# Optimization experiments

Measured on AMD Instinct MI355X. Metric: run time of the kernel, lower is better.

## Reference

```python
import jax, jax.numpy as jnp
import numpy as np

K0, K1, K2, D, DIM, H = 200_000, 600_000, 400_000, 64, 3, 256


def setup_inputs() -> dict:
    key = jax.random.key(0)
    ks = jax.random.split(key, 7)
    dirs = jax.random.normal(ks[0], (D, DIM), dtype=jnp.float32)
    dirs = dirs / jnp.linalg.norm(dirs, axis=1, keepdims=True)  # unit directions
    v_coords = jax.random.normal(ks[1], (K0, DIM), dtype=jnp.float32)
    v_weights = jax.random.uniform(ks[2], (K0,), dtype=jnp.float32)
    edges = jax.random.randint(ks[3], (K1, 2), 0, K0, dtype=jnp.int32)
    e_weights = jax.random.uniform(ks[4], (K1,), dtype=jnp.float32)
    tris = jax.random.randint(ks[5], (K2, 3), 0, K0, dtype=jnp.int32)
    t_weights = jax.random.uniform(ks[6], (K2,), dtype=jnp.float32)
    return dict(v_coords=v_coords, v_weights=v_weights, edges=edges,
                e_weights=e_weights, tris=tris, t_weights=t_weights,
                dirs=dirs, num_heights=H)


def reference(v_coords, v_weights, edges, e_weights, tris, t_weights, dirs, num_heights):
    d = dirs.shape[0]
    h = int(num_heights)
    hf = jnp.asarray(float(h), dtype=v_coords.dtype)
    # vertex height indices per direction: (k0, d)
    max_height = jnp.linalg.norm(v_coords, axis=1).max()
    v_heights = v_coords @ dirs.T
    v_idx = jnp.ceil((hf - 1.0) * (max_height + v_heights) / (2.0 * max_height)).astype(jnp.int32)
    # flattened (d*h,) histogram; per-direction offset folds (dir, height) -> flat bin
    dir_off = (jnp.arange(d, dtype=jnp.int32) * h)[None, :]  # (1, d)
    flat = jnp.zeros((d * h,), dtype=v_weights.dtype)
    # order 0: vertices, sign +1
    flat = flat.at[(v_idx + dir_off).ravel()].add(
        jnp.broadcast_to(v_weights[:, None], v_idx.shape).ravel())
    # order 1: edges, sign (-1)**(1+1) = +1; max vertex index over the 2 endpoints
    e_idx = jnp.max(v_idx[edges], axis=1)  # (k1, d)
    flat = flat.at[(e_idx + dir_off).ravel()].add(
        jnp.broadcast_to(e_weights[:, None], e_idx.shape).ravel())
    # order 2: triangles, sign (-1)**(2+1) = -1; max over the 3 vertices
    t_idx = jnp.max(v_idx[tris], axis=1)  # (k2, d)
    flat = flat.at[(t_idx + dir_off).ravel()].add(
        jnp.broadcast_to(-t_weights[:, None], t_idx.shape).ravel())
    # cumulative sum over heights -> WECT, shape (d, h)
    return jnp.cumsum(flat.reshape(d, h), axis=1)
```

## Files before the change

kernel.cpp:

```cpp
#include <hip/hip_runtime.h>


#define HGT 256
#define NDIR 64
#define NBINS (HGT * NDIR)
#define NG 4
#define GD 16
#define PADH16 258
#define WH16 (GD * PADH16)
#define TPB 192
#define NWV (TPB / 64)
#define VSL 384
#define SSL 384
#define UE 2
#define UT 2
#define UV 2
#define QSCALE 32.0f
#define QINV (1.0f / 32.0f)

__global__ void wect_maxnorm(const float* __restrict__ vc, int k0,
                             unsigned* __restrict__ maxbits) {
    float m = 0.f;
    for (int i = blockIdx.x * blockDim.x + threadIdx.x; i < k0;
         i += gridDim.x * blockDim.x) {
        float x = vc[3 * i], y = vc[3 * i + 1], z = vc[3 * i + 2];
        m = fmaxf(m, sqrtf(x * x + y * y + z * z));
    }
    for (int off = 32; off > 0; off >>= 1)
        m = fmaxf(m, __shfl_down(m, off, 64));
    __shared__ float sm[16];
    int wid = threadIdx.x >> 6, lane = threadIdx.x & 63;
    if (lane == 0) sm[wid] = m;
    __syncthreads();
    if (threadIdx.x == 0) {
        float b = sm[0];
        int nw = blockDim.x >> 6;
        for (int w = 1; w < nw; ++w) b = fmaxf(b, sm[w]);
        atomicMax(maxbits, __float_as_uint(b));
    }
}

__device__ __forceinline__ int height_bin(float h, float mh, float inv) {
    int idx = (int)ceilf((255.0f * (mh + h)) * inv);
    return min(max(idx, 0), HGT - 1);
}

__device__ __forceinline__ int haddr(int dl, int b) {
    int p = ((b & 1) << 7) | (b >> 1);
    return dl * PADH16 + p;
}

__device__ __forceinline__ void flush6(const short* hist, int g,
                                       float* __restrict__ out) {
    for (int t = threadIdx.x; t < GD * HGT; t += TPB) {
        int d = t >> 8, b = t & 255;
        int p = d * PADH16 + (((b & 1) << 7) | (b >> 1));
        int s = 0;
#pragma unroll
        for (int u = 0; u < NWV; ++u) s += (int)hist[u * WH16 + p];
        if (s != 0) atomicAdd(&out[(g * GD + d) * HGT + b], (float)s * QINV);
    }
}

__global__ __launch_bounds__(TPB, 4) void wect_vertex4(
    const float* __restrict__ vc, const float* __restrict__ vw,
    const float* __restrict__ dirs, int k0,
    const unsigned* __restrict__ maxbits, unsigned char* __restrict__ tab,
    float* __restrict__ out) {
    __shared__ short hist[NWV * WH16];
    int tid = threadIdx.x, lane = tid & 63, wv = tid >> 6;
    int dl = lane & 15, sub = lane >> 4;
    for (int t = tid; t < NWV * WH16; t += TPB) hist[t] = 0;
    int g = blockIdx.x & (NG - 1);
    int slice = blockIdx.x >> 2;
    int gd = g * GD + dl;
    float dx = dirs[3 * gd], dy = dirs[3 * gd + 1], dz = dirs[3 * gd + 2];
    float mh = __uint_as_float(*maxbits);
    float inv = 1.0f / (2.0f * mh);
    unsigned char* tabg = tab + (size_t)g * ((size_t)k0 * GD);
    short* H = hist + wv * WH16;
    __syncthreads();
    int lo = (int)((long long)k0 * slice / VSL);
    int hi = (int)((long long)k0 * (slice + 1) / VSL);
    for (int s0 = lo + wv * 4 * UV; s0 < hi; s0 += NWV * 4 * UV) {
        int a_[UV];
        int q_[UV];
#pragma unroll
        for (int u = 0; u < UV; ++u) {
            int s = min(s0 + u * 4 + sub, hi - 1);
            bool act = (s0 + u * 4 + sub) < hi;
            float x = vc[3 * s], y = vc[3 * s + 1], z = vc[3 * s + 2];
            float w = act ? vw[s] : 0.f;
            float h = fmaf(x, dx, fmaf(y, dy, z * dz));
            int b = height_bin(h, mh, inv);
            if (act) tabg[(unsigned)s * GD + dl] = (unsigned char)b;
            a_[u] = haddr(dl, b);
            q_[u] = __float2int_rn(w * QSCALE);
        }
#pragma unroll
        for (int ss = 0; ss < 4; ++ss) {
            if (sub == ss) {
#pragma unroll
                for (int u = 0; u < UV; ++u) {
                    short v = H[a_[u]];
                    H[a_[u]] = (short)(v + q_[u]);
                }
            }
            asm volatile("" ::: "memory");
        }
    }
    __syncthreads();
    flush6(hist, g, out);
}

__global__ __launch_bounds__(TPB, 4) void wect_simplex4(
    const long long* __restrict__ edges, const float* __restrict__ ew,
    const int* __restrict__ tris, const float* __restrict__ tw, int k1, int k2,
    const unsigned char* __restrict__ tab, int k0, float* __restrict__ out) {
    __shared__ short hist[NWV * WH16];
    int tid = threadIdx.x, lane = tid & 63, wv = tid >> 6;
    int dl = lane & 15, sub = lane >> 4;
    for (int t = tid; t < NWV * WH16; t += TPB) hist[t] = 0;
    int g = blockIdx.x & (NG - 1);
    int slice = blockIdx.x >> 2;
    const unsigned char* tabg = tab + (size_t)g * ((size_t)k0 * GD);
    short* H = hist + wv * WH16;
    __syncthreads();

    {
        int lo = (int)((long long)k1 * slice / SSL);
        int hi = (int)((long long)k1 * (slice + 1) / SSL);
        for (int s0 = lo + wv * 4 * UE; s0 < hi; s0 += NWV * 4 * UE) {
            int a_[UE];
            int q_[UE];
#pragma unroll
            for (int u = 0; u < UE; ++u) {
                int s = min(s0 + u * 4 + sub, hi - 1);
                bool act = (s0 + u * 4 + sub) < hi;
                long long ep = edges[s];
                float w = act ? ew[s] : 0.f;
                unsigned ex = (unsigned)(ep & 0xffffffffLL);
                unsigned ey = (unsigned)(ep >> 32);
                int A = tabg[ex * GD + dl];
                int B = tabg[ey * GD + dl];
                a_[u] = haddr(dl, max(A, B));
                q_[u] = __float2int_rn(w * QSCALE);
            }
#pragma unroll
            for (int ss = 0; ss < 4; ++ss) {
                if (sub == ss) {
#pragma unroll
                    for (int u = 0; u < UE; ++u) {
                        short v = H[a_[u]];
                        H[a_[u]] = (short)(v + q_[u]);
                    }
                }
                asm volatile("" ::: "memory");
            }
        }
    }

    {
        int lo = (int)((long long)k2 * slice / SSL);
        int hi = (int)((long long)k2 * (slice + 1) / SSL);
        for (int s0 = lo + wv * 4 * UT; s0 < hi; s0 += NWV * 4 * UT) {
            int a_[UT];
            int q_[UT];
#pragma unroll
            for (int u = 0; u < UT; ++u) {
                int s = min(s0 + u * 4 + sub, hi - 1);
                bool act = (s0 + u * 4 + sub) < hi;
                unsigned i0 = (unsigned)tris[3 * s];
                unsigned i1 = (unsigned)tris[3 * s + 1];
                unsigned i2 = (unsigned)tris[3 * s + 2];
                float w = act ? -tw[s] : 0.f;
                int A = tabg[i0 * GD + dl];
                int B = tabg[i1 * GD + dl];
                int C = tabg[i2 * GD + dl];
                a_[u] = haddr(dl, max(A, max(B, C)));
                q_[u] = __float2int_rn(w * QSCALE);
            }
#pragma unroll
            for (int ss = 0; ss < 4; ++ss) {
                if (sub == ss) {
#pragma unroll
                    for (int u = 0; u < UT; ++u) {
                        short v = H[a_[u]];
                        H[a_[u]] = (short)(v + q_[u]);
                    }
                }
                asm volatile("" ::: "memory");
            }
        }
    }

    __syncthreads();
    flush6(hist, g, out);
}

__global__ void wect_cumsum(float* __restrict__ out) {
    int lane = threadIdx.x;
    float4* row = (float4*)out + (size_t)blockIdx.x * 64;
    float4 v = row[lane];
    v.y += v.x;
    v.z += v.y;
    v.w += v.z;
    float s = v.w;
    float mine = s;
    for (int off = 1; off < 64; off <<= 1) {
        float t = __shfl_up(s, off, 64);
        if (lane >= off) s += t;
    }
    float excl = s - mine;
    v.x += excl;
    v.y += excl;
    v.z += excl;
    v.w += excl;
    row[lane] = v;
}


__global__ __launch_bounds__(512) void wect_simplex_rec(
    const int* __restrict__ edges, const float* __restrict__ ew,
    const int* __restrict__ tris, const float* __restrict__ tw, int k1, int k2,
    const float* __restrict__ vc, const float* __restrict__ dirs,
    const unsigned* __restrict__ maxbits, float* __restrict__ out) {
    __shared__ float hist[NBINS];
    for (int i = threadIdx.x; i < NBINS; i += blockDim.x) hist[i] = 0.f;
    int lane = threadIdx.x & 63;
    float d0 = dirs[lane * 3], d1 = dirs[lane * 3 + 1], d2 = dirs[lane * 3 + 2];
    float mh = __uint_as_float(*maxbits);
    float inv = 1.0f / (2.0f * mh);
    __syncthreads();
    int wid = (blockIdx.x * blockDim.x + threadIdx.x) >> 6;
    int nw = (gridDim.x * blockDim.x) >> 6;
    int total = k1 + k2;
    for (int s = wid; s < total; s += nw) {
        int idx;
        float w;
        if (s < k1) {
            int v0 = edges[2 * s], v1 = edges[2 * s + 1];
            float h0 = vc[3 * v0] * d0 + vc[3 * v0 + 1] * d1 + vc[3 * v0 + 2] * d2;
            float h1 = vc[3 * v1] * d0 + vc[3 * v1 + 1] * d1 + vc[3 * v1 + 2] * d2;
            idx = max(height_bin(h0, mh, inv), height_bin(h1, mh, inv));
            w = ew[s];
        } else {
            int t = s - k1;
            int v0 = tris[3 * t], v1 = tris[3 * t + 1], v2 = tris[3 * t + 2];
            float h0 = vc[3 * v0] * d0 + vc[3 * v0 + 1] * d1 + vc[3 * v0 + 2] * d2;
            float h1 = vc[3 * v1] * d0 + vc[3 * v1 + 1] * d1 + vc[3 * v1 + 2] * d2;
            float h2 = vc[3 * v2] * d0 + vc[3 * v2 + 1] * d1 + vc[3 * v2 + 2] * d2;
            idx = max(height_bin(h0, mh, inv),
                      max(height_bin(h1, mh, inv), height_bin(h2, mh, inv)));
            w = -tw[t];
        }
        atomicAdd(&hist[idx * NDIR + lane], w);
    }
    __syncthreads();
    for (int i = threadIdx.x; i < NBINS; i += blockDim.x) {
        float v = hist[i];
        if (v != 0.f) atomicAdd(&out[(i & 63) * HGT + (i >> 6)], v);
    }
}

__global__ __launch_bounds__(512) void wect_vertex_rec(
    const float* __restrict__ vc, const float* __restrict__ vw,
    const float* __restrict__ dirs, int k0,
    const unsigned* __restrict__ maxbits, float* __restrict__ out) {
    __shared__ float hist[NBINS];
    for (int i = threadIdx.x; i < NBINS; i += blockDim.x) hist[i] = 0.f;
    int lane = threadIdx.x & 63;
    float d0 = dirs[lane * 3], d1 = dirs[lane * 3 + 1], d2 = dirs[lane * 3 + 2];
    float mh = __uint_as_float(*maxbits);
    float inv = 1.0f / (2.0f * mh);
    __syncthreads();
    int wid = (blockIdx.x * blockDim.x + threadIdx.x) >> 6;
    int nw = (gridDim.x * blockDim.x) >> 6;
    for (int k = wid; k < k0; k += nw) {
        float h = vc[3 * k] * d0 + vc[3 * k + 1] * d1 + vc[3 * k + 2] * d2;
        int idx = height_bin(h, mh, inv);
        atomicAdd(&hist[idx * NDIR + lane], vw[k]);
    }
    __syncthreads();
    for (int i = threadIdx.x; i < NBINS; i += blockDim.x) {
        float v = hist[i];
        if (v != 0.f) atomicAdd(&out[(i & 63) * HGT + (i >> 6)], v);
    }
}

extern "C" void kernel_launch(void* const* d_in, const int* in_sizes, int n_in,
                              void* d_out, int out_size, void* d_ws,
                              size_t ws_size, hipStream_t stream) {
    const float* v_coords = (const float*)d_in[0];
    const float* v_weights = (const float*)d_in[1];
    const int* edges = (const int*)d_in[2];
    const float* e_weights = (const float*)d_in[3];
    const int* tris = (const int*)d_in[4];
    const float* t_weights = (const float*)d_in[5];
    const float* dirs = (const float*)d_in[6];

    int k0 = in_sizes[0] / 3;
    int k1 = in_sizes[2] / 2;
    int k2 = in_sizes[4] / 3;

    float* out = (float*)d_out;
    unsigned* maxbits = (unsigned*)d_ws;
    unsigned char* tab = (unsigned char*)d_ws + 64;
    bool have_table = ws_size >= 64 + (size_t)NG * k0 * GD;

    (void)hipMemsetAsync(d_ws, 0, 64, stream);
    (void)hipMemsetAsync(d_out, 0, (size_t)NBINS * sizeof(float), stream);

    wect_maxnorm<<<256, 256, 0, stream>>>(v_coords, k0, maxbits);

    if (have_table) {
        wect_vertex4<<<NG * VSL, TPB, 0, stream>>>(v_coords, v_weights, dirs,
                                                   k0, maxbits, tab, out);
        wect_simplex4<<<NG * SSL, TPB, 0, stream>>>(
            (const long long*)edges, e_weights, tris, t_weights, k1, k2, tab,
            k0, out);
    } else {
        wect_vertex_rec<<<512, 512, 0, stream>>>(v_coords, v_weights, dirs, k0,
                                                 maxbits, out);
        wect_simplex_rec<<<512, 512, 0, stream>>>(edges, e_weights, tris,
                                                  t_weights, k1, k2, v_coords,
                                                  dirs, maxbits, out);
    }
    wect_cumsum<<<NDIR, 64, 0, stream>>>(out);
}
```

Before: 218.9 us.

## Replace serialized sub-group histogram updates with cross-lane dedupe and single update

Each wave holds 4 sub-groups of 16 lanes that can hit the same direction's histogram row. The old code avoided read-modify-write races by taking 4 serialized turns, one per sub-group. The new code uses permlane16/32 swaps (or shfl_xor as a fallback) to find lanes with the same bin address, merges their weights into one lane, and sends the rest to a padding slot. All 64 lanes then do one LDS read-modify-write per element. This trades 4 serialized LDS passes for extra cross-lane VALU work, and relies on the padding column at index 256 to absorb the retired lanes.

```diff
diff --git a/kernel.cpp b/kernel.cpp
--- a/kernel.cpp
+++ b/kernel.cpp
@@ -17,6 +17,45 @@
 #define UV 2
 #define QSCALE 32.0f
 #define QINV (1.0f / 32.0f)
+
+typedef __attribute__((ext_vector_type(2))) unsigned int uint2e;
+
+__device__ __forceinline__ int lxor16(int x, int lane) {
+#if __has_builtin(__builtin_amdgcn_permlane16_swap)
+    uint2e r =
+        __builtin_amdgcn_permlane16_swap((unsigned)x, (unsigned)x, false, false);
+    return (int)((lane & 16) ? r[0] : r[1]);
+#else
+    return __shfl_xor(x, 16, 64);
+#endif
+}
+
+__device__ __forceinline__ int lxor32(int x, int lane) {
+#if __has_builtin(__builtin_amdgcn_permlane32_swap)
+    uint2e r =
+        __builtin_amdgcn_permlane32_swap((unsigned)x, (unsigned)x, false, false);
+    return (int)((lane & 32) ? r[0] : r[1]);
+#else
+    return __shfl_xor(x, 32, 64);
+#endif
+}
+
+__device__ __forceinline__ void dedupe_valu(int& a, int& q, int lane, int pad) {
+    int a16 = lxor16(a, lane), q16 = lxor16(q, lane);
+    int a32 = lxor32(a, lane), q32 = lxor32(q, lane);
+    int a48 = lxor16(a32, lane), q48 = lxor16(q32, lane);
+    bool m16 = (a16 == a), m32 = (a32 == a), m48 = (a48 == a);
+    bool hi16 = (lane & 16) != 0, hi32 = (lane & 32) != 0;
+    bool retired = (m16 && hi16) || ((m32 || m48) && hi32);
+    if (retired) {
+        a = pad;
+        q = 0;
+    } else {
+        if (m16 && !hi16) q += q16;
+        if (m32 && !hi32) q += q32;
+        if (m48 && !hi32) q += q48;
+    }
+}
 
 __global__ void wect_maxnorm(const float* __restrict__ vc, int k0,
                              unsigned* __restrict__ maxbits) {
@@ -79,6 +118,7 @@
     float inv = 1.0f / (2.0f * mh);
     unsigned char* tabg = tab + (size_t)g * ((size_t)k0 * GD);
     short* H = hist + wv * WH16;
+    int pad = dl * PADH16 + 256;
     __syncthreads();
     int lo = (int)((long long)k0 * slice / VSL);
     int hi = (int)((long long)k0 * (slice + 1) / VSL);
@@ -98,15 +138,10 @@
             q_[u] = __float2int_rn(w * QSCALE);
         }
 #pragma unroll
-        for (int ss = 0; ss < 4; ++ss) {
-            if (sub == ss) {
-#pragma unroll
-                for (int u = 0; u < UV; ++u) {
-                    short v = H[a_[u]];
-                    H[a_[u]] = (short)(v + q_[u]);
-                }
-            }
-            asm volatile("" ::: "memory");
+        for (int u = 0; u < UV; ++u) {
+            dedupe_valu(a_[u], q_[u], lane, pad);
+            short v = H[a_[u]];
+            H[a_[u]] = (short)(v + q_[u]);
         }
     }
     __syncthreads();
@@ -125,6 +160,7 @@
     int slice = blockIdx.x >> 2;
     const unsigned char* tabg = tab + (size_t)g * ((size_t)k0 * GD);
     short* H = hist + wv * WH16;
+    int pad = dl * PADH16 + 256;
     __syncthreads();
 
     {
@@ -147,15 +183,10 @@
                 q_[u] = __float2int_rn(w * QSCALE);
             }
 #pragma unroll
-            for (int ss = 0; ss < 4; ++ss) {
-                if (sub == ss) {
-#pragma unroll
-                    for (int u = 0; u < UE; ++u) {
-                        short v = H[a_[u]];
-                        H[a_[u]] = (short)(v + q_[u]);
-                    }
-                }
-                asm volatile("" ::: "memory");
+            for (int u = 0; u < UE; ++u) {
+                dedupe_valu(a_[u], q_[u], lane, pad);
+                short v = H[a_[u]];
+                H[a_[u]] = (short)(v + q_[u]);
             }
         }
     }
@@ -181,15 +212,10 @@
                 q_[u] = __float2int_rn(w * QSCALE);
             }
 #pragma unroll
-            for (int ss = 0; ss < 4; ++ss) {
-                if (sub == ss) {
-#pragma unroll
-                    for (int u = 0; u < UT; ++u) {
-                        short v = H[a_[u]];
-                        H[a_[u]] = (short)(v + q_[u]);
-                    }
-                }
-                asm volatile("" ::: "memory");
+            for (int u = 0; u < UT; ++u) {
+                dedupe_valu(a_[u], q_[u], lane, pad);
+                short v = H[a_[u]];
+                H[a_[u]] = (short)(v + q_[u]);
             }
         }
     }
```

Measured after the change: 221.2 us. About the same (+1.1%).

## Replace serialized sub-group histogram updates with cross-lane duplicate merging

Applied to the files above, without the earlier changes.

Previously, each wave's four 16-lane subgroups updated the shared short histogram one after another to avoid read-modify-write collisions. Now lanes that share a direction compare bin addresses through permlane16/32 swaps (falling back to shuffles). Colliding quantized weights are summed into one owner lane, and the other lanes write zero to a pad slot, so all 64 lanes update the histogram in one pass. A full-chunk fast loop without bounds predicates is also split from a tail loop, at the cost of extra packing and permute instructions per update.

```diff
diff --git a/kernel.cpp b/kernel.cpp
--- a/kernel.cpp
+++ b/kernel.cpp
@@ -17,6 +17,46 @@
 #define UV 2
 #define QSCALE 32.0f
 #define QINV (1.0f / 32.0f)
+
+typedef __attribute__((ext_vector_type(2))) unsigned int uint2e;
+
+__device__ __forceinline__ unsigned pxor16(unsigned x, int lane) {
+#if __has_builtin(__builtin_amdgcn_permlane16_swap)
+    uint2e r = __builtin_amdgcn_permlane16_swap(x, x, false, false);
+    return (lane & 16) ? r[0] : r[1];
+#else
+    return (unsigned)__shfl_xor((int)x, 16, 64);
+#endif
+}
+
+__device__ __forceinline__ unsigned pxor32(unsigned x, int lane) {
+#if __has_builtin(__builtin_amdgcn_permlane32_swap)
+    uint2e r = __builtin_amdgcn_permlane32_swap(x, x, false, false);
+    return (lane & 32) ? r[0] : r[1];
+#else
+    return (unsigned)__shfl_xor((int)x, 32, 64);
+#endif
+}
+
+__device__ __forceinline__ void dedupe_pk(int& a, int& q, int lane, int pad) {
+    unsigned p = ((unsigned)a << 16) | ((unsigned)q & 0xffffu);
+    unsigned p16 = pxor16(p, lane);
+    unsigned p32 = pxor32(p, lane);
+    unsigned p48 = pxor16(p32, lane);
+    bool m16 = ((p ^ p16) >> 16) == 0;
+    bool m32 = ((p ^ p32) >> 16) == 0;
+    bool m48 = ((p ^ p48) >> 16) == 0;
+    bool hi16 = (lane & 16) != 0, hi32 = (lane & 32) != 0;
+    bool retired = (m16 && hi16) || ((m32 || m48) && hi32);
+    if (retired) {
+        a = pad;
+        q = 0;
+    } else {
+        if (m16 && !hi16) q += (short)(p16 & 0xffffu);
+        if (m32 && !hi32) q += (short)(p32 & 0xffffu);
+        if (m48 && !hi32) q += (short)(p48 & 0xffffu);
+    }
+}
 
 __global__ void wect_maxnorm(const float* __restrict__ vc, int k0,
                              unsigned* __restrict__ maxbits) {
@@ -79,12 +119,33 @@
     float inv = 1.0f / (2.0f * mh);
     unsigned char* tabg = tab + (size_t)g * ((size_t)k0 * GD);
     short* H = hist + wv * WH16;
+    int pad = dl * PADH16 + 256;
     __syncthreads();
     int lo = (int)((long long)k0 * slice / VSL);
     int hi = (int)((long long)k0 * (slice + 1) / VSL);
-    for (int s0 = lo + wv * 4 * UV; s0 < hi; s0 += NWV * 4 * UV) {
-        int a_[UV];
-        int q_[UV];
+    int s0 = lo + wv * 4 * UV;
+    for (; s0 + 4 * UV <= hi; s0 += NWV * 4 * UV) {
+        int a_[UV], q_[UV];
+#pragma unroll
+        for (int u = 0; u < UV; ++u) {
+            int s = s0 + u * 4 + sub;
+            float x = vc[3 * s], y = vc[3 * s + 1], z = vc[3 * s + 2];
+            float w = vw[s];
+            float h = fmaf(x, dx, fmaf(y, dy, z * dz));
+            int b = height_bin(h, mh, inv);
+            tabg[(unsigned)s * GD + dl] = (unsigned char)b;
+            a_[u] = haddr(dl, b);
+            q_[u] = __float2int_rn(w * QSCALE);
+        }
+#pragma unroll
+        for (int u = 0; u < UV; ++u) {
+            dedupe_pk(a_[u], q_[u], lane, pad);
+            short v = H[a_[u]];
+            H[a_[u]] = (short)(v + q_[u]);
+        }
+    }
+    for (; s0 < hi; s0 += NWV * 4 * UV) {
+        int a_[UV], q_[UV];
 #pragma unroll
         for (int u = 0; u < UV; ++u) {
             int s = min(s0 + u * 4 + sub, hi - 1);
@@ -95,18 +156,13 @@
             int b = height_bin(h, mh, inv);
             if (act) tabg[(unsigned)s * GD + dl] = (unsigned char)b;
             a_[u] = haddr(dl, b);
-            q_[u] = __float2int_rn(w * QSCALE);
-        }
-#pragma unroll
-        for (int ss = 0; ss < 4; ++ss) {
-            if (sub == ss) {
-#pragma unroll
-                for (int u = 0; u < UV; ++u) {
-                    short v = H[a_[u]];
-                    H[a_[u]] = (short)(v + q_[u]);
-                }
-            }
-            asm volatile("" ::: "memory");
+            q_[u] = act ? __float2int_rn(w * QSCALE) : 0;
+        }
+#pragma unroll
+        for (int u = 0; u < UV; ++u) {
+            dedupe_pk(a_[u], q_[u], lane, pad);
+            short v = H[a_[u]];
+            H[a_[u]] = (short)(v + q_[u]);
         }
     }
     __syncthreads();
@@ -125,14 +181,36 @@
     int slice = blockIdx.x >> 2;
     const unsigned char* tabg = tab + (size_t)g * ((size_t)k0 * GD);
     short* H = hist + wv * WH16;
+    int pad = dl * PADH16 + 256;
     __syncthreads();
 
     {
         int lo = (int)((long long)k1 * slice / SSL);
         int hi = (int)((long long)k1 * (slice + 1) / SSL);
-        for (int s0 = lo + wv * 4 * UE; s0 < hi; s0 += NWV * 4 * UE) {
-            int a_[UE];
-            int q_[UE];
+        int s0 = lo + wv * 4 * UE;
+        for (; s0 + 4 * UE <= hi; s0 += NWV * 4 * UE) {
+            int a_[UE], q_[UE];
+#pragma unroll
+            for (int u = 0; u < UE; ++u) {
+                int s = s0 + u * 4 + sub;
+                long long ep = edges[s];
+                float w = ew[s];
+                unsigned ex = (unsigned)(ep & 0xffffffffLL);
+                unsigned ey = (unsigned)(ep >> 32);
+                int A = tabg[ex * GD + dl];
+                int B = tabg[ey * GD + dl];
+                a_[u] = haddr(dl, max(A, B));
+                q_[u] = __float2int_rn(w * QSCALE);
+            }
+#pragma unroll
+            for (int u = 0; u < UE; ++u) {
+                dedupe_pk(a_[u], q_[u], lane, pad);
+                short v = H[a_[u]];
+                H[a_[u]] = (short)(v + q_[u]);
+            }
+        }
+        for (; s0 < hi; s0 += NWV * 4 * UE) {
+            int a_[UE], q_[UE];
 #pragma unroll
             for (int u = 0; u < UE; ++u) {
                 int s = min(s0 + u * 4 + sub, hi - 1);
@@ -144,18 +222,13 @@
                 int A = tabg[ex * GD + dl];
                 int B = tabg[ey * GD + dl];
                 a_[u] = haddr(dl, max(A, B));
-                q_[u] = __float2int_rn(w * QSCALE);
-            }
-#pragma unroll
-            for (int ss = 0; ss < 4; ++ss) {
-                if (sub == ss) {
-#pragma unroll
-                    for (int u = 0; u < UE; ++u) {
-                        short v = H[a_[u]];
-                        H[a_[u]] = (short)(v + q_[u]);
-                    }
-                }
-                asm volatile("" ::: "memory");
+                q_[u] = act ? __float2int_rn(w * QSCALE) : 0;
+            }
+#pragma unroll
+            for (int u = 0; u < UE; ++u) {
+                dedupe_pk(a_[u], q_[u], lane, pad);
+                short v = H[a_[u]];
+                H[a_[u]] = (short)(v + q_[u]);
             }
         }
     }
@@ -163,9 +236,31 @@
     {
         int lo = (int)((long long)k2 * slice / SSL);
         int hi = (int)((long long)k2 * (slice + 1) / SSL);
-        for (int s0 = lo + wv * 4 * UT; s0 < hi; s0 += NWV * 4 * UT) {
-            int a_[UT];
-            int q_[UT];
+        int s0 = lo + wv * 4 * UT;
+        for (; s0 + 4 * UT <= hi; s0 += NWV * 4 * UT) {
+            int a_[UT], q_[UT];
+#pragma unroll
+            for (int u = 0; u < UT; ++u) {
+                int s = s0 + u * 4 + sub;
+                unsigned i0 = (unsigned)tris[3 * s];
+                unsigned i1 = (unsigned)tris[3 * s + 1];
+                unsigned i2 = (unsigned)tris[3 * s + 2];
+                float w = -tw[s];
+                int A = tabg[i0 * GD + dl];
+                int B = tabg[i1 * GD + dl];
+                int C = tabg[i2 * GD + dl];
+                a_[u] = haddr(dl, max(A, max(B, C)));
+                q_[u] = __float2int_rn(w * QSCALE);
+            }
+#pragma unroll
+            for (int u = 0; u < UT; ++u) {
+                dedupe_pk(a_[u], q_[u], lane, pad);
+                short v = H[a_[u]];
+                H[a_[u]] = (short)(v + q_[u]);
+            }
+        }
+        for (; s0 < hi; s0 += NWV * 4 * UT) {
+            int a_[UT], q_[UT];
 #pragma unroll
             for (int u = 0; u < UT; ++u) {
                 int s = min(s0 + u * 4 + sub, hi - 1);
@@ -178,18 +273,13 @@
                 int B = tabg[i1 * GD + dl];
                 int C = tabg[i2 * GD + dl];
                 a_[u] = haddr(dl, max(A, max(B, C)));
-                q_[u] = __float2int_rn(w * QSCALE);
-            }
-#pragma unroll
-            for (int ss = 0; ss < 4; ++ss) {
-                if (sub == ss) {
-#pragma unroll
-                    for (int u = 0; u < UT; ++u) {
-                        short v = H[a_[u]];
-                        H[a_[u]] = (short)(v + q_[u]);
-                    }
-                }
-                asm volatile("" ::: "memory");
+                q_[u] = act ? __float2int_rn(w * QSCALE) : 0;
+            }
+#pragma unroll
+            for (int u = 0; u < UT; ++u) {
+                dedupe_pk(a_[u], q_[u], lane, pad);
+                short v = H[a_[u]];
+                H[a_[u]] = (short)(v + q_[u]);
             }
         }
     }
```

Result: faster. 189.3 us (-13.5%).
